# Optimization experiments

Measured on AMD Instinct MI355X. Metric: run time of the kernel, lower is better.

The kernel has to match this reference:

```python
import jax, jax.numpy as jnp
import numpy as np
from jax import lax

B, T, U, H, INNER, V = 4, 200, 100, 320, 512, 1000
BLANK = 0


def setup_inputs() -> dict:
    key = jax.random.key(0)
    ks = jax.random.split(key, 8)
    enc_state = jax.random.normal(ks[0], (B, T, H), dtype=jnp.float32)
    dec_state = jax.random.normal(ks[1], (B, U + 1, H), dtype=jnp.float32)
    tokens = jax.random.randint(ks[2], (B, U), 1, V, dtype=jnp.int32)
    output_length = jnp.full((B,), T, dtype=jnp.int32)
    tokens_length = jnp.full((B,), U, dtype=jnp.int32)
    s1 = 1.0 / np.sqrt(2 * H)
    s2 = 1.0 / np.sqrt(INNER)
    W1 = jax.random.uniform(ks[3], (2 * H, INNER), minval=-s1, maxval=s1, dtype=jnp.float32)
    b1 = jax.random.uniform(ks[4], (INNER,), minval=-s1, maxval=s1, dtype=jnp.float32)
    W2 = jax.random.uniform(ks[5], (INNER, V), minval=-s2, maxval=s2, dtype=jnp.float32)
    b2 = jax.random.uniform(ks[6], (V,), minval=-s2, maxval=s2, dtype=jnp.float32)
    return {"enc_state": enc_state, "dec_state": dec_state, "tokens": tokens,
            "output_length": output_length, "tokens_length": tokens_length,
            "W1": W1, "b1": b1, "W2": W2, "b2": b2}


def joint_logits(enc_state, dec_state, W1, b1, W2, b2):
    # concat joint: cat(enc[b,t], dec[b,u]) @ W1 == enc @ W1[:H] + dec @ W1[H:]
    h_enc = jnp.einsum('bth,hi->bti', enc_state, W1[:H])      # (B,T,INNER)
    h_dec = jnp.einsum('buh,hi->bui', dec_state, W1[H:])      # (B,U+1,INNER)
    h = jnp.tanh(h_enc[:, :, None, :] + h_dec[:, None, :, :] + b1)  # (B,T,U+1,INNER)
    return jnp.einsum('btui,iv->btuv', h, W2) + b2            # (B,T,U+1,V)


def rnnt_loss(log_probs, tokens, output_length, tokens_length):
    # log_probs: (B,T,U+1,V); tokens: (B,U) int
    Bn, Tn, U1, _ = log_probs.shape
    blank_lp = log_probs[..., BLANK]                           # (B,T,U+1)
    label_lp = jnp.take_along_axis(
        log_probs[:, :, :U1 - 1, :],
        tokens[:, None, :, None].astype(jnp.int32).repeat(Tn, axis=1),
        axis=-1)[..., 0]                                       # (B,T,U)

    # row t=0: alpha[0,u] = sum_{u'<u} label_lp[0,u']
    def row0_step(c, a):
        n = c + a
        return n, n
    init0 = jnp.zeros((Bn,), dtype=log_probs.dtype)
    _, rest0 = lax.scan(row0_step, init0, label_lp[:, 0, :].T)  # (U,B)
    alpha0 = jnp.concatenate([init0[None], rest0], axis=0).T    # (B,U+1)

    def t_step(alpha_prev, xs):
        blank_prev, label_t = xs                # (B,U+1), (B,U)
        b = alpha_prev + blank_prev             # blank transition from row t-1
        def u_step(c, inp):
            b_u, a_prev = inp
            n = jnp.logaddexp(b_u, c + a_prev)
            return n, n
        first = b[:, 0]
        _, rest = lax.scan(u_step, first, (b[:, 1:].T, label_t.T))
        alpha_t = jnp.concatenate([first[None], rest], axis=0).T
        return alpha_t, alpha_t

    xs = (blank_lp[:, :-1, :].transpose(1, 0, 2), label_lp[:, 1:, :].transpose(1, 0, 2))
    _, alphas = lax.scan(t_step, alpha0, xs)                    # (T-1,B,U+1)
    alpha = jnp.concatenate([alpha0[None], alphas], axis=0).transpose(1, 0, 2)  # (B,T,U+1)

    bidx = jnp.arange(Bn)
    t_idx = output_length - 1
    u_idx = tokens_length
    ll = alpha[bidx, t_idx, u_idx] + blank_lp[bidx, t_idx, u_idx]
    return -jnp.mean(ll)


def reference(enc_state, dec_state, tokens, output_length, tokens_length, W1, b1, W2, b2):
    logits = joint_logits(enc_state, dec_state, W1, b1, W2, b2)
    log_probs = jax.nn.log_softmax(logits, axis=-1)
    return rnnt_loss(log_probs, tokens, output_length, tokens_length)
```

## Files before the change

### kernel.cpp

```cpp
#include <hip/hip_runtime.h>
#include <hip/hip_bf16.h>

#define T_DIM 200
#define U_DIM 100
#define U1    101
#define H_DIM 320
#define K_INNER 512
#define V_DIM 1000
#define B_DIM 4
#define ND 300
#define ROWS 48
#define XPITCH 520
#define CHUNK 8

typedef unsigned short ushort_t;
typedef unsigned char uchar_t;
typedef unsigned int uint32;
typedef long lfrag;

typedef float ffrag4 __attribute__((ext_vector_type(4)));

#define LOG2E   1.4426950408889634f
#define LOG2E16 (1.4426950408889634f * 0.0625f)
#define LN2     0.6931471805599453f

__device__ __forceinline__ float tanh_fast(float x) {
  float e = __expf(2.0f * x);
  return 1.0f - __fdividef(2.0f, e + 1.0f);
}

__device__ __forceinline__ uint2 pk_fp8x8(float t0, float t1, float t2, float t3,
                                          float t4, float t5, float t6, float t7) {
  uint2 r;
  r.x = (uint32)__builtin_amdgcn_cvt_pk_fp8_f32(t0, t1, 0, false);
  r.x = (uint32)__builtin_amdgcn_cvt_pk_fp8_f32(t2, t3, (int)r.x, true);
  r.y = (uint32)__builtin_amdgcn_cvt_pk_fp8_f32(t4, t5, 0, false);
  r.y = (uint32)__builtin_amdgcn_cvt_pk_fp8_f32(t6, t7, (int)r.y, true);
  return r;
}

__device__ __forceinline__ float dpp_up1(float v, float oldv) {
  return __int_as_float(__builtin_amdgcn_update_dpp(
      __float_as_int(oldv), __float_as_int(v), 0x138, 0xf, 0xf, false));
}

__global__ __launch_bounds__(512)
void prep_kernel(const float* __restrict__ enc, const float* __restrict__ dec,
                 const float* __restrict__ W1, const float* __restrict__ W2,
                 float* __restrict__ hEnc, float* __restrict__ hDec,
                 uchar_t* __restrict__ W2f8)
{
  __shared__ union { float sIn[8][H_DIM]; float sW[8][1024]; } sh;
  const int tid = threadIdx.x;
  const int blk = blockIdx.x;

  if (blk < 151) {
    const float* inp; float* outp; int nRows, rowOff, b0;
    if (blk < 100) { inp = enc; outp = hEnc; nRows = B_DIM * T_DIM; rowOff = 0;     b0 = blk; }
    else           { inp = dec; outp = hDec; nRows = B_DIM * U1;    rowOff = H_DIM; b0 = blk - 100; }
    const int r0 = b0 * 8;
    for (int i = tid; i < 8 * H_DIM; i += 512) {
      int r = i / H_DIM, k = i - r * H_DIM;
      int rr = r0 + r;
      sh.sIn[r][k] = (rr < nRows) ? inp[(size_t)rr * H_DIM + k] : 0.0f;
    }
    __syncthreads();
    const int c = tid;
    float acc[8];
#pragma unroll
    for (int r = 0; r < 8; ++r) acc[r] = 0.0f;
    const float* Wp = W1 + (size_t)rowOff * K_INNER + c;
    for (int k = 0; k < H_DIM; k += 4) {
      float w0 = Wp[(size_t)(k + 0) * K_INNER];
      float w1 = Wp[(size_t)(k + 1) * K_INNER];
      float w2 = Wp[(size_t)(k + 2) * K_INNER];
      float w3 = Wp[(size_t)(k + 3) * K_INNER];
#pragma unroll
      for (int r = 0; r < 8; ++r) {
        float4 s = *(const float4*)&sh.sIn[r][k];
        acc[r] = fmaf(s.w, w3, fmaf(s.z, w2, fmaf(s.y, w1, fmaf(s.x, w0, acc[r]))));
      }
    }
#pragma unroll
    for (int r = 0; r < 8; ++r) {
      int rr = r0 + r;
      if (rr < nRows) outp[(size_t)rr * K_INNER + c] = acc[r];
    }
  } else {
    const int kc = blk - 151;
    for (int i = tid; i < 8 * 1024; i += 512) {
      int r = i >> 10, n = i & 1023;
      sh.sW[r][n] = (n < V_DIM) ? W2[(size_t)(kc * 8 + r) * V_DIM + n] : 0.0f;
    }
    __syncthreads();
    const int ks = kc >> 2, q = kc & 3;
#pragma unroll
    for (int h = 0; h < 2; ++h) {
      int n = tid + h * 512;
      uint2 pk = pk_fp8x8(sh.sW[0][n] * 16.f, sh.sW[1][n] * 16.f,
                          sh.sW[2][n] * 16.f, sh.sW[3][n] * 16.f,
                          sh.sW[4][n] * 16.f, sh.sW[5][n] * 16.f,
                          sh.sW[6][n] * 16.f, sh.sW[7][n] * 16.f);
      const int ct = n >> 8, w = (n >> 6) & 3, col = n & 63;
      const size_t off = (size_t)(ct * 16 + ks) * 8192 + w * 2048 + q * 512 + col * 8;
      *(uint2*)&W2f8[off] = pk;
    }
  }
}

__global__ __launch_bounds__(256, 3)
void joint_kernel(const float* __restrict__ hEnc, const float* __restrict__ hDec,
                  const float* __restrict__ b1, const uchar_t* __restrict__ W2f8,
                  const float* __restrict__ b2, const int* __restrict__ tokens,
                  float* __restrict__ pD)
{
  __shared__ union SU {
    uchar_t X[ROWS * XPITCH];
    float red[4][ROWS][4];
  } sh;
  __shared__ __align__(16) uchar_t sB[4][2][2048];

  const int tid = threadIdx.x;
  const int b  = blockIdx.z;
  const int t0 = blockIdx.y * 12;
  const int u0 = blockIdx.x * 4;
  const int wave = tid >> 6;
  const int lane = tid & 63;
  const int l15 = lane & 15;
  const int quad = lane >> 4;

  float b2s[4][4];
#pragma unroll
  for (int ct = 0; ct < 4; ++ct)
#pragma unroll
    for (int cb = 0; cb < 4; ++cb) {
      int v = ct * 256 + wave * 64 + cb * 16 + l15;
      b2s[ct][cb] = (v < V_DIM) ? b2[v] * LOG2E : -1e30f;
    }
  int tokv[4];
#pragma unroll
  for (int j = 0; j < 4; ++j)
    tokv[j] = (u0 + j < U_DIM) ? tokens[b * U_DIM + u0 + j] : -1;

  for (int i = tid; i < ROWS * 64; i += 256) {
    const int row = i >> 6;
    const int G = i & 63;
    const int tcl = min(t0 + (row >> 2), T_DIM - 1);
    const int ucl = min(u0 + (row & 3), U1 - 1);
    const float* er = hEnc + (size_t)(b * T_DIM + tcl) * K_INNER;
    const float* dr = hDec + (size_t)(b * U1 + ucl) * K_INNER;
    const int k = G << 3;
    float4 e0 = *(const float4*)(er + k);
    float4 e1 = *(const float4*)(er + k + 4);
    float4 d0 = *(const float4*)(dr + k);
    float4 d1 = *(const float4*)(dr + k + 4);
    float4 c0 = *(const float4*)(b1 + k);
    float4 c1 = *(const float4*)(b1 + k + 4);
    uint2 pk = pk_fp8x8(tanh_fast(e0.x + d0.x + c0.x), tanh_fast(e0.y + d0.y + c0.y),
                        tanh_fast(e0.z + d0.z + c0.z), tanh_fast(e0.w + d0.w + c0.w),
                        tanh_fast(e1.x + d1.x + c1.x), tanh_fast(e1.y + d1.y + c1.y),
                        tanh_fast(e1.z + d1.z + c1.z), tanh_fast(e1.w + d1.w + c1.w));
    *(uint2*)&sh.X[row * XPITCH + (G << 3)] = pk;
  }
  __syncthreads();

  uchar_t* sBw = &sB[wave][0][0];
  const uchar_t* gW = W2f8 + (size_t)wave * 2048 + (size_t)lane * 16;

#define STAGE(gbase, bufv)                                                          \
  {                                                                                 \
    __builtin_amdgcn_global_load_lds(                                               \
        (const __attribute__((address_space(1))) void*)(gbase),                     \
        (__attribute__((address_space(3))) void*)(sBw + (bufv) * 2048), 16, 0, 0);  \
    __builtin_amdgcn_global_load_lds(                                               \
        (const __attribute__((address_space(1))) void*)((gbase) + 1024),            \
        (__attribute__((address_space(3))) void*)(sBw + (bufv) * 2048 + 1024), 16, 0, 0); \
  }

  STAGE(gW, 0)
  const uchar_t* gP = gW + 8192;

  const uchar_t* aB = &sh.X[l15 * XPITCH + quad * 8];
  const uchar_t* bL = sBw + quad * 512 + l15 * 8;

  float sumexp[3][4], labelA[3][4], blankV[3][4];
#pragma unroll
  for (int i = 0; i < 3; ++i)
#pragma unroll
    for (int j = 0; j < 4; ++j) { sumexp[i][j] = 0.0f; labelA[i][j] = 0.0f; blankV[i][j] = 0.0f; }

#pragma unroll 1
  for (int ct = 0; ct < 4; ++ct) {
    ffrag4 acc[3][4];
    ffrag4 zero4 = {0.0f, 0.0f, 0.0f, 0.0f};
#pragma unroll
    for (int rb = 0; rb < 3; ++rb)
#pragma unroll
      for (int cb = 0; cb < 4; ++cb) acc[rb][cb] = zero4;

#pragma unroll
    for (int ks = 0; ks < 16; ++ks) {
      if (ks < 15 || ct < 3) {
        STAGE(gP, (ks + 1) & 1)
        gP += 8192;
        asm volatile("s_waitcnt vmcnt(2)" ::: "memory");
      } else {
        asm volatile("s_waitcnt vmcnt(0)" ::: "memory");
      }
      lfrag av[3];
#pragma unroll
      for (int rb = 0; rb < 3; ++rb)
        av[rb] = *(const lfrag*)(aB + rb * (16 * XPITCH) + ks * 32);
      lfrag bv[4];
#pragma unroll
      for (int cb = 0; cb < 4; ++cb)
        bv[cb] = *(const lfrag*)(bL + (ks & 1) * 2048 + cb * 128);
#pragma unroll
      for (int rb = 0; rb < 3; ++rb)
#pragma unroll
        for (int cb = 0; cb < 4; ++cb)
          acc[rb][cb] = __builtin_amdgcn_mfma_f32_16x16x32_fp8_fp8(av[rb], bv[cb], acc[rb][cb], 0, 0, 0);
    }

#pragma unroll
    for (int cb = 0; cb < 4; ++cb) {
      const int v = ct * 256 + wave * 64 + cb * 16 + l15;
      const float bs = b2s[ct][cb];
#pragma unroll
      for (int rb = 0; rb < 3; ++rb)
#pragma unroll
        for (int reg = 0; reg < 4; ++reg) {
          float a = acc[rb][cb][reg];
          sumexp[rb][reg] += exp2f(fmaf(a, LOG2E16, bs));
          labelA[rb][reg] += (v == tokv[reg]) ? a : 0.0f;
        }
    }
    if (ct == 0 && wave == 0) {
#pragma unroll
      for (int rb = 0; rb < 3; ++rb)
#pragma unroll
        for (int reg = 0; reg < 4; ++reg) blankV[rb][reg] = acc[rb][0][reg];
    }
  }
#undef STAGE

#pragma unroll
  for (int mask = 1; mask <= 8; mask <<= 1) {
#pragma unroll
    for (int rb = 0; rb < 3; ++rb)
#pragma unroll
      for (int reg = 0; reg < 4; ++reg) {
        sumexp[rb][reg] += __shfl_xor(sumexp[rb][reg], mask, 64);
        labelA[rb][reg] += __shfl_xor(labelA[rb][reg], mask, 64);
      }
  }

  __syncthreads();
  if (l15 == 0) {
#pragma unroll
    for (int rb = 0; rb < 3; ++rb)
#pragma unroll
      for (int reg = 0; reg < 4; ++reg) {
        int row = rb * 16 + quad * 4 + reg;
        sh.red[wave][row][0] = sumexp[rb][reg];
        sh.red[wave][row][1] = blankV[rb][reg];
        sh.red[wave][row][2] = labelA[rb][reg];
      }
  }
  __syncthreads();
  if (tid < ROWS) {
    float S  = sh.red[0][tid][0] + sh.red[1][tid][0] + sh.red[2][tid][0] + sh.red[3][tid][0];
    float Bl = sh.red[0][tid][1] + sh.red[1][tid][1] + sh.red[2][tid][1] + sh.red[3][tid][1];
    float Lb = sh.red[0][tid][2] + sh.red[1][tid][2] + sh.red[2][tid][2] + sh.red[3][tid][2];
    int t = t0 + (tid >> 2);
    int u = u0 + (tid & 3);
    if (t < T_DIM && u < U1) {
      float lse2 = __log2f(S);
      int tok = (u < U_DIM) ? tokens[b * U_DIM + u] : 0;
      int d = t + u;
      size_t idx = (((size_t)b * ND + d) * 128 + u) * 2;
      pD[idx]     = fmaf(Bl, LOG2E16, b2[0]   * LOG2E) - lse2;
      pD[idx + 1] = fmaf(Lb, LOG2E16, b2[tok] * LOG2E) - lse2;
    }
  }
}

__global__ __launch_bounds__(256)
void dp_kernel(const float* __restrict__ pD,
               const int* __restrict__ outLen, const int* __restrict__ tokLen,
               float* __restrict__ outLoss)
{
  __shared__ __align__(16) float sD[4][3][CHUNK * 256];
  __shared__ float llsh[B_DIM];
  const int tid = threadIdx.x;
  const int wv = tid >> 6;
  const int lane = tid & 63;
  const float* src = pD + (size_t)wv * ND * 256;
  const int tIdx = outLen[wv] - 1;
  const int uIdx = tokLen[wv];
  const int dStar = tIdx + uIdx;
  const float NEG = -1e30f;
  const float blkStar = src[((size_t)dStar * 128 + uIdx) * 2];

  float aE = (lane == 0) ? 0.0f : NEG;
  float aO = NEG;
  float ll2 = 0.0f;
  if (dStar == 0 && lane == 0) ll2 = blkStar;

  const int uE = 2 * lane;

#define ISSUE(c, buf)                                                         \
  {                                                                           \
    const float* g_ = src + (size_t)(c) * (CHUNK * 256);                      \
    float* l_ = &sD[wv][(buf)][0];                                            \
    _Pragma("unroll")                                                         \
    for (int j_ = 0; j_ < CHUNK; ++j_)                                        \
      __builtin_amdgcn_global_load_lds(                                       \
        (const __attribute__((address_space(1))) void*)(g_ + j_ * 256 + lane * 4), \
        (__attribute__((address_space(3))) void*)(l_ + j_ * 256), 16, 0, 0);  \
  }

  ISSUE(0, 0)
  ISSUE(1, 1)
#pragma unroll 1
  for (int c = 0; c < 38; ++c) {
    { const int nc = c + 2; const int cc = nc <= 37 ? nc : 37; ISSUE(cc, nc % 3) }
    asm volatile("s_waitcnt vmcnt(16)" ::: "memory");
    const float* buf = &sD[wv][c % 3][0];
    float4 qv[CHUNK];
#pragma unroll
    for (int j = 0; j < CHUNK; ++j)
      qv[j] = *(const float4*)&buf[j * 256 + uE * 2];
#pragma unroll
    for (int j = 0; j < CHUNK; ++j) {
      const int d = c * CHUNK + 1 + j;
      float4 q = qv[j];
      float aO_up = dpp_up1(aO, NEG);
      float labUp = dpp_up1(q.w, NEG);
      float bt0 = aE + q.x, lt0 = aO_up + labUp;
      float mx0 = fmaxf(bt0, lt0), mn0 = fminf(bt0, lt0);
      float r0 = mx0 + __log2f(1.0f + exp2f(mn0 - mx0));
      int te = d - uE;
      float nE = ((uE <= U_DIM) && (te >= 0) && (te < T_DIM)) ? r0 : NEG;
      float bt1 = aO + q.z, lt1 = aE + q.y;
      float mx1 = fmaxf(bt1, lt1), mn1 = fminf(bt1, lt1);
      float r1 = mx1 + __log2f(1.0f + exp2f(mn1 - mx1));
      int to = te - 1;
      float nO = ((uE + 1 <= U_DIM) && (to >= 0) && (to < T_DIM)) ? r1 : NEG;
      aE = nE; aO = nO;
      if (d == dStar) {
        if (uIdx == uE)          ll2 = nE + blkStar;
        else if (uIdx == uE + 1) ll2 = nO + blkStar;
      }
    }
  }
#undef ISSUE

#pragma unroll
  for (int mask = 1; mask < 64; mask <<= 1) ll2 += __shfl_xor(ll2, mask, 64);
  if (lane == 0) llsh[wv] = ll2;
  __syncthreads();
  if (tid == 0)
    outLoss[0] = -(llsh[0] + llsh[1] + llsh[2] + llsh[3]) * 0.25f * LN2;
}

extern "C" void kernel_launch(void* const* d_in, const int* in_sizes, int n_in,
                              void* d_out, int out_size, void* d_ws, size_t ws_size,
                              hipStream_t stream)
{
  const float* enc    = (const float*)d_in[0];
  const float* dec    = (const float*)d_in[1];
  const int*   tokens = (const int*)d_in[2];
  const int*   outLen = (const int*)d_in[3];
  const int*   tokLen = (const int*)d_in[4];
  const float* W1     = (const float*)d_in[5];
  const float* b1     = (const float*)d_in[6];
  const float* W2     = (const float*)d_in[7];
  const float* b2     = (const float*)d_in[8];
  float* out = (float*)d_out;

  char* ws = (char*)d_ws;
  float*   hEnc = (float*)(ws + 0);
  float*   hDec = (float*)(ws + 1638400);
  uchar_t* W2f8 = (uchar_t*)(ws + 2465792);
  float*   pD   = (float*)(ws + 2990080);

  prep_kernel<<<dim3(215), dim3(512), 0, stream>>>(enc, dec, W1, W2, hEnc, hDec, W2f8);
  joint_kernel<<<dim3(26, 17, B_DIM), dim3(256), 0, stream>>>(hEnc, hDec, b1, W2f8, b2, tokens, pD);
  dp_kernel<<<dim3(1), dim3(256), 0, stream>>>(pD, outLen, tokLen, out);
}
```

Baseline: 258.8 us.

## Switch joint GEMM to 16x16x128 scaled FP8 MFMA with register-prefetched B

Replaces the 16x16x32 FP8 MFMA with the MI355X scaled 16x16x128 f8f6f4 MFMA, using unit scales, so each instruction covers four times the K depth. The W2 FP8 pre-pack layout is reorganised so every lane can load its 32-byte B fragment directly from global memory into registers, with double buffering. This removes the LDS staging buffer for B and its global_load_lds path. The ct loop is fully unrolled and launch bounds drop to 2 blocks per SM, trading occupancy for the extra register pressure of the double-buffered fragments.

```diff
diff --git a/kernel.cpp b/kernel.cpp
--- a/kernel.cpp
+++ b/kernel.cpp
@@ -19,6 +19,7 @@
 typedef long lfrag;
 
 typedef float ffrag4 __attribute__((ext_vector_type(4)));
+typedef int   ifrag  __attribute__((ext_vector_type(8)));
 
 #define LOG2E   1.4426950408889634f
 #define LOG2E16 (1.4426950408889634f * 0.0625f)
@@ -93,7 +94,7 @@
       sh.sW[r][n] = (n < V_DIM) ? W2[(size_t)(kc * 8 + r) * V_DIM + n] : 0.0f;
     }
     __syncthreads();
-    const int ks = kc >> 2, q = kc & 3;
+    const int ks4 = kc >> 4, qd = (kc >> 2) & 3, part = (kc >> 1) & 1, io = (kc & 1) * 8;
 #pragma unroll
     for (int h = 0; h < 2; ++h) {
       int n = tid + h * 512;
@@ -101,14 +102,15 @@
                           sh.sW[2][n] * 16.f, sh.sW[3][n] * 16.f,
                           sh.sW[4][n] * 16.f, sh.sW[5][n] * 16.f,
                           sh.sW[6][n] * 16.f, sh.sW[7][n] * 16.f);
-      const int ct = n >> 8, w = (n >> 6) & 3, col = n & 63;
-      const size_t off = (size_t)(ct * 16 + ks) * 8192 + w * 2048 + q * 512 + col * 8;
+      const int ct = n >> 8, w = (n >> 6) & 3, cb = (n >> 4) & 3, l15 = n & 15;
+      const int R = ct * 64 + ks4 * 16 + w * 4 + cb;
+      const size_t off = (size_t)R * 2048 + part * 1024 + (qd * 16 + l15) * 16 + io;
       *(uint2*)&W2f8[off] = pk;
     }
   }
 }
 
-__global__ __launch_bounds__(256, 3)
+__global__ __launch_bounds__(256, 2)
 void joint_kernel(const float* __restrict__ hEnc, const float* __restrict__ hDec,
                   const float* __restrict__ b1, const uchar_t* __restrict__ W2f8,
                   const float* __restrict__ b2, const int* __restrict__ tokens,
@@ -118,7 +120,6 @@
     uchar_t X[ROWS * XPITCH];
     float red[4][ROWS][4];
   } sh;
-  __shared__ __align__(16) uchar_t sB[4][2][2048];
 
   const int tid = threadIdx.x;
   const int b  = blockIdx.z;
@@ -128,6 +129,19 @@
   const int lane = tid & 63;
   const int l15 = lane & 15;
   const int quad = lane >> 4;
+
+  const uchar_t* gB = W2f8 + (size_t)wave * 8192 + (size_t)lane * 16;
+  ifrag bv[2][4];
+
+#define LOADB(g_, s_)                                                        \
+  {                                                                          \
+    _Pragma("unroll")                                                        \
+    for (int cb_ = 0; cb_ < 4; ++cb_) {                                      \
+      const uchar_t* p_ = gB + (size_t)((g_) * 16 + cb_) * 2048;             \
+      *(int4*)&bv[s_][cb_]       = *(const int4*)p_;                         \
+      *((int4*)&bv[s_][cb_] + 1) = *(const int4*)(p_ + 1024);                \
+    }                                                                        \
+  }
 
   float b2s[4][4];
 #pragma unroll
@@ -162,26 +176,11 @@
                         tanh_fast(e1.z + d1.z + c1.z), tanh_fast(e1.w + d1.w + c1.w));
     *(uint2*)&sh.X[row * XPITCH + (G << 3)] = pk;
   }
+
+  LOADB(0, 0)
   __syncthreads();
 
-  uchar_t* sBw = &sB[wave][0][0];
-  const uchar_t* gW = W2f8 + (size_t)wave * 2048 + (size_t)lane * 16;
-
-#define STAGE(gbase, bufv)                                                          \
-  {                                                                                 \
-    __builtin_amdgcn_global_load_lds(                                               \
-        (const __attribute__((address_space(1))) void*)(gbase),                     \
-        (__attribute__((address_space(3))) void*)(sBw + (bufv) * 2048), 16, 0, 0);  \
-    __builtin_amdgcn_global_load_lds(                                               \
-        (const __attribute__((address_space(1))) void*)((gbase) + 1024),            \
-        (__attribute__((address_space(3))) void*)(sBw + (bufv) * 2048 + 1024), 16, 0, 0); \
-  }
-
-  STAGE(gW, 0)
-  const uchar_t* gP = gW + 8192;
-
-  const uchar_t* aB = &sh.X[l15 * XPITCH + quad * 8];
-  const uchar_t* bL = sBw + quad * 512 + l15 * 8;
+  const uchar_t* aB = &sh.X[l15 * XPITCH + quad * 32];
 
   float sumexp[3][4], labelA[3][4], blankV[3][4];
 #pragma unroll
@@ -189,7 +188,9 @@
 #pragma unroll
     for (int j = 0; j < 4; ++j) { sumexp[i][j] = 0.0f; labelA[i][j] = 0.0f; blankV[i][j] = 0.0f; }
 
-#pragma unroll 1
+  union AF { ifrag f; lfrag q[4]; };
+
+#pragma unroll
   for (int ct = 0; ct < 4; ++ct) {
     ffrag4 acc[3][4];
     ffrag4 zero4 = {0.0f, 0.0f, 0.0f, 0.0f};
@@ -199,27 +200,30 @@
       for (int cb = 0; cb < 4; ++cb) acc[rb][cb] = zero4;
 
 #pragma unroll
-    for (int ks = 0; ks < 16; ++ks) {
-      if (ks < 15 || ct < 3) {
-        STAGE(gP, (ks + 1) & 1)
-        gP += 8192;
-        asm volatile("s_waitcnt vmcnt(2)" ::: "memory");
-      } else {
-        asm volatile("s_waitcnt vmcnt(0)" ::: "memory");
-      }
-      lfrag av[3];
+    for (int ks4 = 0; ks4 < 4; ++ks4) {
+      const int g = ct * 4 + ks4;
+      const int slot = ks4 & 1;
+      if (g < 15) LOADB(g + 1, slot ^ 1)
+      AF av[3];
+#pragma unroll
+      for (int rb = 0; rb < 3; ++rb) {
+        const uchar_t* ap = aB + rb * (16 * XPITCH) + ks4 * 128;
+        av[rb].q[0] = *(const lfrag*)(ap);
+        av[rb].q[1] = *(const lfrag*)(ap + 8);
+        av[rb].q[2] = *(const lfrag*)(ap + 16);
+        av[rb].q[3] = *(const lfrag*)(ap + 24);
+      }
+      if (g < 15) { asm volatile("s_waitcnt vmcnt(8)" ::: "memory"); }
+      else        { asm volatile("s_waitcnt vmcnt(0)" ::: "memory"); }
 #pragma unroll
       for (int rb = 0; rb < 3; ++rb)
-        av[rb] = *(const lfrag*)(aB + rb * (16 * XPITCH) + ks * 32);
-      lfrag bv[4];
-#pragma unroll
-      for (int cb = 0; cb < 4; ++cb)
-        bv[cb] = *(const lfrag*)(bL + (ks & 1) * 2048 + cb * 128);
-#pragma unroll
-      for (int rb = 0; rb < 3; ++rb)
 #pragma unroll
         for (int cb = 0; cb < 4; ++cb)
-          acc[rb][cb] = __builtin_amdgcn_mfma_f32_16x16x32_fp8_fp8(av[rb], bv[cb], acc[rb][cb], 0, 0, 0);
+          acc[rb][cb] = __builtin_amdgcn_mfma_scale_f32_16x16x128_f8f6f4(
+              av[rb].f, bv[slot][cb], acc[rb][cb],
+              0, 0,
+              0, 0x7f7f7f7f,
+              0, 0x7f7f7f7f);
     }
 
 #pragma unroll
@@ -242,7 +246,7 @@
         for (int reg = 0; reg < 4; ++reg) blankV[rb][reg] = acc[rb][0][reg];
     }
   }
-#undef STAGE
+#undef LOADB
 
 #pragma unroll
   for (int mask = 1; mask <= 8; mask <<= 1) {
```

Measured after the change: 246.9 us. 4.6% less time.
